# Kernel tuning notes

Hardware: AMD Instinct MI355X
Metric: run time of the kernel (lower is better)

## Reference

```python
import jax, jax.numpy as jnp
import numpy as np
from jax import lax

D = 512        # datapathSize (= slow-net hidden size = embedding size)
H = 20         # nonlinearAfterSlowHiddenSize
V = 32000      # softmaxOutputHeadSize = xEmbeddingsNum
T = 1024       # sequence length (number of sequential fast-weight updates)


def setup_inputs() -> dict:
    key = jax.random.key(0)
    ks = jax.random.split(key, 12)
    inp = {}
    inp["tokens"] = jax.random.randint(ks[0], (T,), 0, V)
    inp["targets"] = jax.random.randint(ks[1], (T,), 0, V)
    # learned parameters
    inp["embed"] = jax.random.normal(ks[2], (V, D), dtype=jnp.float32)
    # fastWeightsInit = rand(D,D) * (1/D)
    inp["fw_init"] = jax.random.uniform(ks[3], (D, D), dtype=jnp.float32) * (1.0 / D)
    inp["eta"] = jnp.array(1.0, dtype=jnp.float32)
    inp["wa"] = jax.random.normal(ks[4], (D, D), dtype=jnp.float32) * 0.05
    inp["wb"] = jax.random.normal(ks[5], (D, D), dtype=jnp.float32) * 0.05
    # nonlinearAfterSlow: Linear(D,H) -> selu -> Linear(H,D); stored as (in,out)
    lim_a = 1.0 / np.sqrt(D)
    inp["mlp_aw"] = jax.random.uniform(ks[6], (D, H), dtype=jnp.float32, minval=-lim_a, maxval=lim_a)
    inp["mlp_ab"] = jax.random.uniform(ks[7], (H,), dtype=jnp.float32, minval=-lim_a, maxval=lim_a)
    lim_b = 1.0 / np.sqrt(H)
    inp["mlp_bw"] = jax.random.uniform(ks[8], (H, D), dtype=jnp.float32, minval=-lim_b, maxval=lim_b)
    inp["mlp_bb"] = jax.random.uniform(ks[9], (D,), dtype=jnp.float32, minval=-lim_b, maxval=lim_b)
    # logit head Linear(D, V)
    inp["head_w"] = jax.random.uniform(ks[10], (D, V), dtype=jnp.float32, minval=-lim_a, maxval=lim_a)
    inp["head_b"] = jax.random.uniform(ks[11], (V,), dtype=jnp.float32, minval=-lim_a, maxval=lim_a)
    return inp


def reference(tokens, targets, embed, fw_init, eta, wa, wb,
              mlp_aw, mlp_ab, mlp_bw, mlp_bb, head_w, head_b):
    xs = embed[tokens]  # [T, D]

    def step(fw, x):
        # SlowNetB.forwardAndUpdate for one token
        z0 = x @ wa                      # [D]
        z1 = x @ wb                      # [D]
        fw_new = jnp.tanh(fw + eta * jnp.outer(z0, z1))  # [D, D]
        y = x @ fw_new                   # [D]
        return fw_new, y

    _, ys = lax.scan(step, fw_init, xs)  # ys: [T, D]

    # NonlinearLayer (batched over T)
    h = jax.nn.selu(ys @ mlp_aw + mlp_ab) @ mlp_bw + mlp_bb  # [T, D]
    mixed = 0.5 * h + 0.5 * xs
    logits = mixed @ head_w + head_b     # [T, V]

    logp = jax.nn.log_softmax(logits, axis=-1)
    loss = -jnp.mean(jnp.take_along_axis(logp, targets[:, None], axis=1))
    return logits, loss
```

## Files before the change

### kernel.cpp

```cpp
#include <hip/hip_runtime.h>

#define D 512
#define H 20
#define V 32000
#define T 1024
#define NT2 500
#define NPART 16

typedef unsigned int uint;
typedef __attribute__((ext_vector_type(8))) short short8;
typedef __attribute__((ext_vector_type(4))) float floatx4;

#define CC 2.8853900817779268f
#define M2C -5.7707801635558537f

__device__ __forceinline__ unsigned short f2bf(float f) {
    unsigned u = __builtin_bit_cast(unsigned, f);
    u += 0x7fffu + ((u >> 16) & 1u);
    return (unsigned short)(u >> 16);
}

template <int CTRL>
__device__ __forceinline__ float dpp_add(float v) {
    int x = __builtin_amdgcn_update_dpp(0, __builtin_bit_cast(int, v), CTRL, 0xf, 0xf, true);
    return v + __builtin_bit_cast(float, x);
}
template <int CTRL>
__device__ __forceinline__ float dpp_max(float v) {
    int x = __builtin_amdgcn_update_dpp(0, __builtin_bit_cast(int, v), CTRL, 0xf, 0xf, true);
    return fmaxf(v, __builtin_bit_cast(float, x));
}
__device__ __forceinline__ float reduce16(float v) {
    v = dpp_add<0xB1>(v);
    v = dpp_add<0x4E>(v);
    v = dpp_add<0x141>(v);
    v = dpp_add<0x140>(v);
    return v;
}
__device__ __forceinline__ float reduce16max(float v) {
    v = dpp_max<0xB1>(v);
    v = dpp_max<0x4E>(v);
    v = dpp_max<0x141>(v);
    v = dpp_max<0x140>(v);
    return v;
}

__global__ __launch_bounds__(256) void gather_kernel(const int* __restrict__ tokens,
                                                     const float* __restrict__ embed,
                                                     float* __restrict__ xs,
                                                     float* __restrict__ loss_acc) {
    int idx = blockIdx.x * 256 + threadIdx.x;
    if (idx == 0) *loss_acc = 0.f;
    int row = idx >> 7;
    int c   = idx & 127;
    float4 v = ((const float4*)(embed + (long)tokens[row] * D))[c];
    ((float4*)xs)[idx] = v;
}

__global__ __launch_bounds__(256) void zgemm_kernel(const float* __restrict__ xs,
                                                    const float* __restrict__ wa,
                                                    const float* __restrict__ wb,
                                                    const float* __restrict__ eta_p,
                                                    float* __restrict__ z0,
                                                    float* __restrict__ z1) {
    __shared__ float Xs[16 * 36];
    __shared__ float Ws[16 * 68];
    const int tid = threadIdx.x;
    const int n0 = blockIdx.x * 64, m0 = blockIdx.y * 32;
    const float* Wm = blockIdx.z ? wb : wa;
    float* Z = blockIdx.z ? z1 : z0;
    const float sc = blockIdx.z ? 1.0f : (*eta_p) * CC;
    const int tx = tid & 15, ty = tid >> 4;
    const int xr = tid >> 3, xk = (tid & 7) * 2;
    const int wr = tid >> 4, wc = (tid & 15) * 4;
    float acc[2][4] = {};
    for (int k0 = 0; k0 < D; k0 += 16) {
        float2 xv = *(const float2*)(xs + (m0 + xr) * D + k0 + xk);
        float4 wv = *(const float4*)(Wm + (k0 + wr) * D + n0 + wc);
        Xs[(xk + 0) * 36 + xr] = xv.x;
        Xs[(xk + 1) * 36 + xr] = xv.y;
        *(float4*)(Ws + wr * 68 + wc) = wv;
        __syncthreads();
#pragma unroll
        for (int k = 0; k < 16; k++) {
            float a0 = Xs[k * 36 + 2 * ty];
            float a1 = Xs[k * 36 + 2 * ty + 1];
            float4 b = *(const float4*)(Ws + k * 68 + tx * 4);
            float bv[4] = {b.x, b.y, b.z, b.w};
#pragma unroll
            for (int c = 0; c < 4; c++) {
                acc[0][c] = __builtin_fmaf(a0, bv[c], acc[0][c]);
                acc[1][c] = __builtin_fmaf(a1, bv[c], acc[1][c]);
            }
        }
        __syncthreads();
    }
    float4 v0 = {sc * acc[0][0], sc * acc[0][1], sc * acc[0][2], sc * acc[0][3]};
    float4 v1 = {sc * acc[1][0], sc * acc[1][1], sc * acc[1][2], sc * acc[1][3]};
    *(float4*)(Z + (m0 + 2 * ty + 0) * D + n0 + tx * 4) = v0;
    *(float4*)(Z + (m0 + 2 * ty + 1) * D + n0 + tx * 4) = v1;
}

#define LOADC(B, tbase)                                                       \
    {                                                                         \
        _Pragma("unroll")                                                     \
        for (int c = 0; c < 8; c++) {                                         \
            const int tr = ((tbase) + c) * D;                                 \
            za##B[c] = *(const float2*)(z0 + tr + i0);                        \
            xa##B[c] = *(const float2*)(xs + tr + i0);                        \
            ez##B[c] = z1[tr + j];                                            \
        }                                                                     \
    }

#define COMPUTE(B, tbase)                                                     \
    {                                                                         \
        float p[8];                                                           \
        _Pragma("unroll")                                                     \
        for (int c = 0; c < 8; c++) {                                         \
            float e = ez##B[c];                                               \
            float a0 = __builtin_amdgcn_exp2f(__builtin_fmaf(e, za##B[c].x, g0)); \
            float a1 = __builtin_amdgcn_exp2f(__builtin_fmaf(e, za##B[c].y, g1)); \
            float r0 = __builtin_amdgcn_rcpf(a0 + 1.0f);                      \
            float r1 = __builtin_amdgcn_rcpf(a1 + 1.0f);                      \
            g0 = __builtin_fmaf(M2C, r0, CC);                                 \
            g1 = __builtin_fmaf(M2C, r1, CC);                                 \
            p[c] = __builtin_fmaf(xa##B[c].y, g1, xa##B[c].x * g0);           \
        }                                                                     \
        _Pragma("unroll")                                                     \
        for (int c = 0; c < 8; c++) p[c] = reduce16(p[c]);                    \
        if ((lane & 15) == 0) {                                               \
            _Pragma("unroll")                                                 \
            for (int c = 0; c < 8; c++) yp[((tbase) + c) * D] = p[c];         \
        }                                                                     \
    }

__global__ __launch_bounds__(64) void scan_kernel(const float* __restrict__ z0,
                                                  const float* __restrict__ z1,
                                                  const float* __restrict__ xs,
                                                  const float* __restrict__ fw_init,
                                                  float* __restrict__ ypart) {
    const int lane = threadIdx.x;
    const int bid = blockIdx.x;
    const int j = bid & 511;
    const int q = bid >> 9;
    const int i0 = q * 128 + 2 * lane;
    float g0 = CC * fw_init[(long)i0 * D + j];
    float g1 = CC * fw_init[(long)(i0 + 1) * D + j];
    float* yp = ypart + ((long)(q * 4 + (lane >> 4)) * T) * D + j;

    float2 zaA[8], xaA[8], zaB[8], xaB[8];
    float  ezA[8], ezB[8];

    LOADC(A, 0);
    for (int t0 = 0; t0 < T; t0 += 16) {
        LOADC(B, t0 + 8);
        COMPUTE(A, t0);
        if (t0 + 16 < T) { LOADC(A, t0 + 16); }
        COMPUTE(B, t0 + 8);
    }
}

__global__ __launch_bounds__(256) void mlp_fused_kernel(const float* __restrict__ ypart,
                                                        const float* __restrict__ xs,
                                                        const float* __restrict__ Aw,
                                                        const float* __restrict__ Ab,
                                                        const float* __restrict__ Bw,
                                                        const float* __restrict__ Bb,
                                                        unsigned short* __restrict__ mixed) {
    const int t = blockIdx.x, tid = threadIdx.x;
    __shared__ float y_lds[D];
    __shared__ float h_lds[H];
    const float INVC = 0.34657359027997264f;
#pragma unroll
    for (int s = 0; s < 2; s++) {
        int d = s * 256 + tid;
        float v = 0.f;
#pragma unroll
        for (int qq = 0; qq < NPART; qq++)
            v += __builtin_nontemporal_load(ypart + ((long)qq * T + t) * D + d);
        y_lds[d] = v * INVC;
    }
    __syncthreads();
    const int w = tid >> 6, lane = tid & 63;
    float yv[8];
#pragma unroll
    for (int k = 0; k < 8; k++) yv[k] = y_lds[k * 64 + lane];
#pragma unroll
    for (int u = 0; u < 5; u++) {
        const int jj = w * 5 + u;
        float a = 0.f;
#pragma unroll
        for (int k = 0; k < 8; k++)
            a = __builtin_fmaf(yv[k], Aw[(k * 64 + lane) * H + jj], a);
        a = reduce16(a);
        a += __shfl_xor(a, 16, 64);
        a += __shfl_xor(a, 32, 64);
        if (lane == 0) {
            a += Ab[jj];
            const float sc = 1.0507009873554805f, al = 1.6732632423543772f;
            h_lds[jj] = a > 0.f ? sc * a : sc * al * (__expf(a) - 1.f);
        }
    }
    __syncthreads();
#pragma unroll
    for (int s = 0; s < 2; s++) {
        int d = s * 256 + tid;
        float o = Bb[d];
#pragma unroll
        for (int jj = 0; jj < H; jj++) o = __builtin_fmaf(h_lds[jj], Bw[jj * D + d], o);
        int gi = t * D + d;
        mixed[gi] = f2bf(0.5f * o + 0.5f * xs[gi]);
    }
}

__global__ __launch_bounds__(256) void convert_wt_kernel(const float* __restrict__ head_w,
                                                         unsigned short* __restrict__ wt) {
    __shared__ float tile[64 * 68];
    const int n0 = blockIdx.x * 64, k0 = blockIdx.y * 64;
    const int tid = threadIdx.x;
#pragma unroll
    for (int s = 0; s < 4; s++) {
        int idx4 = s * 256 + tid;
        int r = idx4 >> 4, c4 = idx4 & 15;
        float4 v = *(const float4*)(head_w + (long)(k0 + r) * V + n0 + c4 * 4);
        *(float4*)(tile + r * 68 + c4 * 4) = v;
    }
    __syncthreads();
    const int rr = tid >> 2;
    const int cq = tid & 3;
    uint u[8];
#pragma unroll
    for (int p = 0; p < 8; p++) {
        float a = tile[(cq * 16 + p * 2 + 0) * 68 + rr];
        float b = tile[(cq * 16 + p * 2 + 1) * 68 + rr];
        u[p] = (uint)f2bf(a) | ((uint)f2bf(b) << 16);
    }
    unsigned short* ob = wt + (long)(n0 + rr) * D + k0 + cq * 16;
    uint4 v0 = {u[0], u[1], u[2], u[3]};
    uint4 v1 = {u[4], u[5], u[6], u[7]};
    *(uint4*)ob = v0;
    *((uint4*)ob + 1) = v1;
}

__global__ __launch_bounds__(256) void head_gemm_kernel(const unsigned short* __restrict__ A,
                                                        const unsigned short* __restrict__ Bt,
                                                        const float* __restrict__ bias,
                                                        float* __restrict__ C,
                                                        float* __restrict__ pm,
                                                        float* __restrict__ ps) {
    __shared__ unsigned short As[128 * 64];
    __shared__ unsigned short Bs[128 * 64];
    const int tid = threadIdx.x;
    const int mt = blockIdx.x & 7, nt = blockIdx.x >> 3;
    const int m0 = mt * 128, n0 = nt * 128;
    const int wave = tid >> 6, lane = tid & 63;
    const int wm = wave >> 1, wn = wave & 1;
    const int quad = lane >> 4, l15 = lane & 15;
    floatx4 acc[4][4] = {};
    for (int k0 = 0; k0 < D; k0 += 64) {
#pragma unroll
        for (int s = 0; s < 4; s++) {
            int idx = s * 256 + tid;
            int row = idx >> 3, slot = idx & 7;
            int gch = slot ^ (row & 7);
            const unsigned short* ga = A + (long)(m0 + row) * D + k0 + gch * 8;
            __builtin_amdgcn_global_load_lds(
                (const __attribute__((address_space(1))) unsigned int*)ga,
                (__attribute__((address_space(3))) unsigned int*)(As + idx * 8), 16, 0, 0);
            const unsigned short* gb = Bt + (long)(n0 + row) * D + k0 + gch * 8;
            __builtin_amdgcn_global_load_lds(
                (const __attribute__((address_space(1))) unsigned int*)gb,
                (__attribute__((address_space(3))) unsigned int*)(Bs + idx * 8), 16, 0, 0);
        }
        __syncthreads();
#pragma unroll
        for (int ks = 0; ks < 2; ks++) {
            short8 af[4], bfr[4];
            int q = ks * 4 + quad;
#pragma unroll
            for (int f = 0; f < 4; f++) {
                int ar = wm * 64 + f * 16 + l15;
                af[f] = *(const short8*)(As + ar * 64 + ((q ^ (ar & 7)) * 8));
                int br = wn * 64 + f * 16 + l15;
                bfr[f] = *(const short8*)(Bs + br * 64 + ((q ^ (br & 7)) * 8));
            }
#pragma unroll
            for (int fr = 0; fr < 4; fr++)
#pragma unroll
                for (int fc = 0; fc < 4; fc++)
                    acc[fr][fc] = __builtin_amdgcn_mfma_f32_16x16x32_bf16(af[fr], bfr[fc],
                                                                          acc[fr][fc], 0, 0, 0);
        }
        __syncthreads();
    }
    float bv[4];
#pragma unroll
    for (int fc = 0; fc < 4; fc++) bv[fc] = bias[n0 + wn * 64 + fc * 16 + l15];
#pragma unroll
    for (int fr = 0; fr < 4; fr++) {
        int mr = m0 + wm * 64 + fr * 16 + quad * 4;
#pragma unroll
        for (int r = 0; r < 4; r++) {
            float v[4];
#pragma unroll
            for (int fc = 0; fc < 4; fc++) {
                v[fc] = acc[fr][fc][r] + bv[fc];
                C[(long)(mr + r) * V + n0 + wn * 64 + fc * 16 + l15] = v[fc];
            }
            float mx = fmaxf(fmaxf(v[0], v[1]), fmaxf(v[2], v[3]));
            mx = reduce16max(mx);
            float sv = __expf(v[0] - mx) + __expf(v[1] - mx)
                     + __expf(v[2] - mx) + __expf(v[3] - mx);
            sv = reduce16(sv);
            if (l15 == 0) {
                long row = mr + r;
                pm[row * NT2 + nt * 2 + wn] = mx;
                ps[row * NT2 + nt * 2 + wn] = sv;
            }
        }
    }
}

__device__ __forceinline__ void lse_comb(float& m, float& s, float m2, float s2) {
    float M = fmaxf(m, m2);
    s = s * __expf(m - M) + s2 * __expf(m2 - M);
    m = M;
}

__global__ __launch_bounds__(256) void loss_rows_kernel(const float* __restrict__ pm,
                                                        const float* __restrict__ ps,
                                                        const float* __restrict__ logits,
                                                        const int* __restrict__ targets,
                                                        float* __restrict__ loss_acc) {
    const int t = blockIdx.x, tid = threadIdx.x;
    float m = -INFINITY, s = 0.f;
    for (int i = tid; i < NT2; i += 256)
        lse_comb(m, s, pm[(long)t * NT2 + i], ps[(long)t * NT2 + i]);
#pragma unroll
    for (int msk = 1; msk <= 32; msk <<= 1) {
        float m2 = __shfl_xor(m, msk, 64);
        float s2 = __shfl_xor(s, msk, 64);
        lse_comb(m, s, m2, s2);
    }
    __shared__ float sm[4], ss[4];
    if ((tid & 63) == 0) { sm[tid >> 6] = m; ss[tid >> 6] = s; }
    __syncthreads();
    if (tid == 0) {
        float M = sm[0], S = ss[0];
#pragma unroll
        for (int w = 1; w < 4; w++) lse_comb(M, S, sm[w], ss[w]);
        float lse = M + __logf(S);
        float lt = logits[(long)t * V + targets[t]];
        atomicAdd(loss_acc, (lse - lt) * (1.0f / (float)T));
    }
}

extern "C" void kernel_launch(void* const* d_in, const int* in_sizes, int n_in,
                              void* d_out, int out_size, void* d_ws, size_t ws_size,
                              hipStream_t stream) {
    const int*   tokens  = (const int*)d_in[0];
    const int*   targets = (const int*)d_in[1];
    const float* embed   = (const float*)d_in[2];
    const float* fw_init = (const float*)d_in[3];
    const float* eta     = (const float*)d_in[4];
    const float* wa      = (const float*)d_in[5];
    const float* wb      = (const float*)d_in[6];
    const float* mlp_aw  = (const float*)d_in[7];
    const float* mlp_ab  = (const float*)d_in[8];
    const float* mlp_bw  = (const float*)d_in[9];
    const float* mlp_bb  = (const float*)d_in[10];
    const float* head_w  = (const float*)d_in[11];
    const float* head_b  = (const float*)d_in[12];
    float* out = (float*)d_out;
    float* loss_acc = out + (long)T * V;

    char* ws = (char*)d_ws;
    float*          xs      = (float*)(ws + 0);
    float*          z0      = (float*)(ws + 2097152);
    float*          z1      = (float*)(ws + 4194304);
    float*          ypart   = (float*)(ws + 6291456);
    unsigned short* wt      = (unsigned short*)(ws + 2097152);
    float*          pm      = (float*)(ws + 0);
    float*          psum    = (float*)(ws + 37748736);
    unsigned short* mixed   = (unsigned short*)(ws + 39845888);

    gather_kernel<<<(T * D / 4) / 256, 256, 0, stream>>>(tokens, embed, xs, loss_acc);
    zgemm_kernel<<<dim3(D / 64, T / 32, 2), 256, 0, stream>>>(xs, wa, wb, eta, z0, z1);
    scan_kernel<<<2048, 64, 0, stream>>>(z0, z1, xs, fw_init, ypart);
    mlp_fused_kernel<<<T, 256, 0, stream>>>(ypart, xs, mlp_aw, mlp_ab, mlp_bw, mlp_bb, mixed);
    convert_wt_kernel<<<dim3(V / 64, D / 64), 256, 0, stream>>>(head_w, wt);
    head_gemm_kernel<<<(T / 128) * (V / 128), 256, 0, stream>>>(mixed, wt, head_b, out, pm, psum);
    loss_rows_kernel<<<T, 256, 0, stream>>>(pm, psum, out, targets, loss_acc);
}
```

Baseline: 548.9 us.

## Reduce scan partials across full wavefront and remap blocks by XCD

The scan kernel now does a full 64-lane reduction (DPP plus cross-row shuffles), so it writes 4 partial-sum planes instead of 16, and the MLP kernel reads 4 planes instead of 16. Each lane now handles rows i and i+64 with scalar loads instead of adjacent float2 pairs. Block indices are remapped so blocks sharing the same row quarter land on the same XCD, which should improve L2 reuse of the z0/xs rows. The loss atomic is replaced by per-row writes plus a final single-block reduction kernel, making it deterministic at the cost of one extra launch. The extra shuffles sit on the serial scan path.

```diff
diff --git a/kernel.cpp b/kernel.cpp
--- a/kernel.cpp
+++ b/kernel.cpp
@@ -5,7 +5,6 @@
 #define V 32000
 #define T 1024
 #define NT2 500
-#define NPART 16
 
 typedef unsigned int uint;
 typedef __attribute__((ext_vector_type(8))) short short8;
@@ -47,10 +46,8 @@
 
 __global__ __launch_bounds__(256) void gather_kernel(const int* __restrict__ tokens,
                                                      const float* __restrict__ embed,
-                                                     float* __restrict__ xs,
-                                                     float* __restrict__ loss_acc) {
+                                                     float* __restrict__ xs) {
     int idx = blockIdx.x * 256 + threadIdx.x;
-    if (idx == 0) *loss_acc = 0.f;
     int row = idx >> 7;
     int c   = idx & 127;
     float4 v = ((const float4*)(embed + (long)tokens[row] * D))[c];
@@ -101,15 +98,17 @@
     *(float4*)(Z + (m0 + 2 * ty + 1) * D + n0 + tx * 4) = v1;
 }
 
-#define LOADC(B, tbase)                                                       \
-    {                                                                         \
-        _Pragma("unroll")                                                     \
-        for (int c = 0; c < 8; c++) {                                         \
-            const int tr = ((tbase) + c) * D;                                 \
-            za##B[c] = *(const float2*)(z0 + tr + i0);                        \
-            xa##B[c] = *(const float2*)(xs + tr + i0);                        \
-            ez##B[c] = z1[tr + j];                                            \
-        }                                                                     \
+#define LOADC(B, tbase)                                        \
+    {                                                          \
+        _Pragma("unroll")                                      \
+        for (int c = 0; c < 8; c++) {                          \
+            const int tr = ((tbase) + c) * D;                  \
+            za##B[c] = z0[tr + i0];                            \
+            zb##B[c] = z0[tr + i1];                            \
+            xa##B[c] = xs[tr + i0];                            \
+            xb##B[c] = xs[tr + i1];                            \
+            ez##B[c] = z1[tr + j];                             \
+        }                                                      \
     }
 
 #define COMPUTE(B, tbase)                                                     \
@@ -118,17 +117,22 @@
         _Pragma("unroll")                                                     \
         for (int c = 0; c < 8; c++) {                                         \
             float e = ez##B[c];                                               \
-            float a0 = __builtin_amdgcn_exp2f(__builtin_fmaf(e, za##B[c].x, g0)); \
-            float a1 = __builtin_amdgcn_exp2f(__builtin_fmaf(e, za##B[c].y, g1)); \
+            float a0 = __builtin_amdgcn_exp2f(__builtin_fmaf(e, za##B[c], g0)); \
+            float a1 = __builtin_amdgcn_exp2f(__builtin_fmaf(e, zb##B[c], g1)); \
             float r0 = __builtin_amdgcn_rcpf(a0 + 1.0f);                      \
             float r1 = __builtin_amdgcn_rcpf(a1 + 1.0f);                      \
             g0 = __builtin_fmaf(M2C, r0, CC);                                 \
             g1 = __builtin_fmaf(M2C, r1, CC);                                 \
-            p[c] = __builtin_fmaf(xa##B[c].y, g1, xa##B[c].x * g0);           \
+            p[c] = xa##B[c] * g0 + xb##B[c] * g1;                             \
         }                                                                     \
         _Pragma("unroll")                                                     \
-        for (int c = 0; c < 8; c++) p[c] = reduce16(p[c]);                    \
-        if ((lane & 15) == 0) {                                               \
+        for (int c = 0; c < 8; c++) {                                         \
+            float v = reduce16(p[c]);                                         \
+            v += __shfl_xor(v, 16, 64);                                       \
+            v += __shfl_xor(v, 32, 64);                                       \
+            p[c] = v;                                                         \
+        }                                                                     \
+        if (lane == 0) {                                                      \
             _Pragma("unroll")                                                 \
             for (int c = 0; c < 8; c++) yp[((tbase) + c) * D] = p[c];         \
         }                                                                     \
@@ -141,16 +145,17 @@
                                                   float* __restrict__ ypart) {
     const int lane = threadIdx.x;
     const int bid = blockIdx.x;
-    const int j = bid & 511;
-    const int q = bid >> 9;
-    const int i0 = q * 128 + 2 * lane;
+    const int xcd = bid & 7, idx = bid >> 3;
+    const int q = xcd >> 1;
+    const int j = (idx << 1) | (xcd & 1);
+    const int i0 = q * 128 + lane;
+    const int i1 = i0 + 64;
     float g0 = CC * fw_init[(long)i0 * D + j];
-    float g1 = CC * fw_init[(long)(i0 + 1) * D + j];
-    float* yp = ypart + ((long)(q * 4 + (lane >> 4)) * T) * D + j;
-
-    float2 zaA[8], xaA[8], zaB[8], xaB[8];
-    float  ezA[8], ezB[8];
-
+    float g1 = CC * fw_init[(long)i1 * D + j];
+    float* yp = ypart + (long)q * T * D + j;
+
+    float zaA[8], zbA[8], xaA[8], xbA[8], ezA[8];
+    float zaB[8], zbB[8], xaB[8], xbB[8], ezB[8];
     LOADC(A, 0);
     for (int t0 = 0; t0 < T; t0 += 16) {
         LOADC(B, t0 + 8);
@@ -174,10 +179,8 @@
 #pragma unroll
     for (int s = 0; s < 2; s++) {
         int d = s * 256 + tid;
-        float v = 0.f;
-#pragma unroll
-        for (int qq = 0; qq < NPART; qq++)
-            v += __builtin_nontemporal_load(ypart + ((long)qq * T + t) * D + d);
+        float v = ypart[(0 * T + t) * D + d] + ypart[(1 * T + t) * D + d]
+                + ypart[(2 * T + t) * D + d] + ypart[(3 * T + t) * D + d];
         y_lds[d] = v * INVC;
     }
     __syncthreads();
@@ -331,7 +334,7 @@
                                                         const float* __restrict__ ps,
                                                         const float* __restrict__ logits,
                                                         const int* __restrict__ targets,
-                                                        float* __restrict__ loss_acc) {
+                                                        float* __restrict__ ws_loss) {
     const int t = blockIdx.x, tid = threadIdx.x;
     float m = -INFINITY, s = 0.f;
     for (int i = tid; i < NT2; i += 256)
@@ -351,8 +354,21 @@
         for (int w = 1; w < 4; w++) lse_comb(M, S, sm[w], ss[w]);
         float lse = M + __logf(S);
         float lt = logits[(long)t * V + targets[t]];
-        atomicAdd(loss_acc, (lse - lt) * (1.0f / (float)T));
-    }
+        ws_loss[t] = lse - lt;
+    }
+}
+
+__global__ __launch_bounds__(256) void loss_final_kernel(const float* __restrict__ ws_loss,
+                                                         float* __restrict__ out) {
+    const int tid = threadIdx.x;
+    float s = 0.f;
+    for (int i = tid; i < T; i += 256) s += ws_loss[i];
+#pragma unroll
+    for (int m = 1; m <= 32; m <<= 1) s += __shfl_xor(s, m, 64);
+    __shared__ float red[4];
+    if ((tid & 63) == 0) red[tid >> 6] = s;
+    __syncthreads();
+    if (tid == 0) out[0] = (red[0] + red[1] + red[2] + red[3]) * (1.f / (float)T);
 }
 
 extern "C" void kernel_launch(void* const* d_in, const int* in_sizes, int n_in,
@@ -372,7 +388,6 @@
     const float* head_w  = (const float*)d_in[11];
     const float* head_b  = (const float*)d_in[12];
     float* out = (float*)d_out;
-    float* loss_acc = out + (long)T * V;
 
     char* ws = (char*)d_ws;
     float*          xs      = (float*)(ws + 0);
@@ -380,15 +395,17 @@
     float*          z1      = (float*)(ws + 4194304);
     float*          ypart   = (float*)(ws + 6291456);
     unsigned short* wt      = (unsigned short*)(ws + 2097152);
+    unsigned short* mixed   = (unsigned short*)(ws + 36700160);
     float*          pm      = (float*)(ws + 0);
     float*          psum    = (float*)(ws + 37748736);
-    unsigned short* mixed   = (unsigned short*)(ws + 39845888);
-
-    gather_kernel<<<(T * D / 4) / 256, 256, 0, stream>>>(tokens, embed, xs, loss_acc);
+    float*          ws_loss = (float*)(ws + 39845888);
+
+    gather_kernel<<<(T * D / 4) / 256, 256, 0, stream>>>(tokens, embed, xs);
     zgemm_kernel<<<dim3(D / 64, T / 32, 2), 256, 0, stream>>>(xs, wa, wb, eta, z0, z1);
     scan_kernel<<<2048, 64, 0, stream>>>(z0, z1, xs, fw_init, ypart);
     mlp_fused_kernel<<<T, 256, 0, stream>>>(ypart, xs, mlp_aw, mlp_ab, mlp_bw, mlp_bb, mixed);
     convert_wt_kernel<<<dim3(V / 64, D / 64), 256, 0, stream>>>(head_w, wt);
     head_gemm_kernel<<<(T / 128) * (V / 128), 256, 0, stream>>>(mixed, wt, head_b, out, pm, psum);
-    loss_rows_kernel<<<T, 256, 0, stream>>>(pm, psum, out, targets, loss_acc);
-}
+    loss_rows_kernel<<<T, 256, 0, stream>>>(pm, psum, out, targets, ws_loss);
+    loss_final_kernel<<<1, 256, 0, stream>>>(ws_loss, out + (long)T * V);
+}
```

Result: faster. 518.9 us (-5.5%).
